# Performance work log

Hardware: AMD Instinct MI355X
Metric: run time of the kernel (lower is better)

Reference implementation:

```python
import jax, jax.numpy as jnp
import numpy as np

DIM = 4096
N_HEADS = 32
HEAD_DIM = DIM // N_HEADS  # 128
BSZ = 2
SEQLEN = 2048


def setup_inputs() -> dict:
    key = jax.random.key(0)
    ks = jax.random.split(key, 8)
    x = jax.random.normal(ks[0], (BSZ, SEQLEN, DIM), dtype=jnp.float32)
    # rotary frequencies (LLaMA): theta = 10000^{-2i/d}, angle = pos * theta
    inv_freq = 1.0 / (10000.0 ** (np.arange(0, HEAD_DIM, 2, dtype=np.float32) / HEAD_DIM))
    angles = np.arange(SEQLEN, dtype=np.float32)[:, None] * inv_freq[None, :]  # [S, hd/2]
    freqs_cos = jnp.asarray(np.cos(angles))
    freqs_sin = jnp.asarray(np.sin(angles))
    # causal additive mask [1,1,S,S]
    neg = jnp.float32(-1e9)
    mask = jnp.where(jnp.tril(jnp.ones((SEQLEN, SEQLEN), dtype=bool)), 0.0, neg)[None, None]
    scale = 0.02
    wq = jax.random.normal(ks[1], (DIM, DIM), dtype=jnp.float32) * scale
    wk = jax.random.normal(ks[2], (DIM, DIM), dtype=jnp.float32) * scale
    wv = jax.random.normal(ks[3], (DIM, DIM), dtype=jnp.float32) * scale
    wo = jax.random.normal(ks[4], (DIM, DIM), dtype=jnp.float32) * scale
    return {"x": x, "start_pos": 0, "freqs_cos": freqs_cos, "freqs_sin": freqs_sin,
            "mask": mask, "wq": wq, "wk": wk, "wv": wv, "wo": wo}


def _apply_rotary(t, cos, sin):
    # t: [B,S,H,hd]; cos/sin: [S,hd/2] -> broadcast [1,S,1,hd/2]
    t = t.reshape(*t.shape[:-1], HEAD_DIM // 2, 2)
    t0, t1 = t[..., 0], t[..., 1]
    c = cos[None, :, None, :]
    s = sin[None, :, None, :]
    r0 = t0 * c - t1 * s
    r1 = t0 * s + t1 * c
    return jnp.stack([r0, r1], axis=-1).reshape(*t0.shape[:-1], HEAD_DIM)


def reference(x, start_pos, freqs_cos, freqs_sin, mask, wq, wk, wv, wo):
    bsz, seqlen, _ = x.shape
    # QKV projections (nn.Linear: y = x @ W.T; weights stored [out,in])
    xq = (x @ wq.T).reshape(bsz, seqlen, N_HEADS, HEAD_DIM)
    xk = (x @ wk.T).reshape(bsz, seqlen, N_HEADS, HEAD_DIM)
    xv = (x @ wv.T).reshape(bsz, seqlen, N_HEADS, HEAD_DIM)
    xq = _apply_rotary(xq, freqs_cos, freqs_sin)
    xk = _apply_rotary(xk, freqs_cos, freqs_sin)
    # [B,H,S,hd]
    q = xq.transpose(0, 2, 1, 3)
    k = xk.transpose(0, 2, 1, 3)
    v = xv.transpose(0, 2, 1, 3)
    scale = 1.0 / jnp.sqrt(jnp.float32(HEAD_DIM))
    scores = jnp.einsum('bhqd,bhkd->bhqk', q, k) * scale + mask
    probs = jax.nn.softmax(scores, axis=-1)
    out = jnp.einsum('bhqk,bhkd->bhqd', probs, v)  # [B,H,S,hd]
    out = out.transpose(0, 2, 1, 3).reshape(bsz, seqlen, DIM)
    return out @ wo.T
```

## Files before the change

kernel.cpp:

```cpp
#include <hip/hip_runtime.h>

typedef unsigned short ushort_t;
typedef unsigned int u32;
typedef short bf16x8 __attribute__((ext_vector_type(8)));
typedef float f32x4 __attribute__((ext_vector_type(4)));
typedef float f32x16 __attribute__((ext_vector_type(16)));
typedef u32 u32x4 __attribute__((ext_vector_type(4)));

__device__ __forceinline__ ushort_t f2bf(float f) {
  u32 u = __builtin_bit_cast(u32, f);
  u += 0x7FFFu + ((u >> 16) & 1u);
  return (ushort_t)(u >> 16);
}
__device__ __forceinline__ float bf2f(u32 bits16) {
  return __builtin_bit_cast(float, bits16 << 16);
}

__global__ __launch_bounds__(256)
void cvt_kernel(const float* __restrict__ in, ushort_t* __restrict__ out) {
  const int i = blockIdx.x * 256 + threadIdx.x;
  const float4 a = ((const float4*)in)[(size_t)i * 2];
  const float4 b = ((const float4*)in)[(size_t)i * 2 + 1];
  uint4 r;
  r.x = (u32)f2bf(a.x) | ((u32)f2bf(a.y) << 16);
  r.y = (u32)f2bf(a.z) | ((u32)f2bf(a.w) << 16);
  r.z = (u32)f2bf(b.x) | ((u32)f2bf(b.y) << 16);
  r.w = (u32)f2bf(b.z) | ((u32)f2bf(b.w) << 16);
  ((uint4*)out)[i] = r;
}

template <int F32OUT>
__global__ __launch_bounds__(512, 2)
void gemm256(const ushort_t* __restrict__ A, const ushort_t* __restrict__ B,
             void* __restrict__ C) {
  constexpr int KD = 4096, ND = 4096;
  __shared__ ushort_t sA[2][2][128 * 64];
  __shared__ ushort_t sB[2][2][128 * 64];
  const int tid = threadIdx.x;
  const int lane = tid & 63, wave = tid >> 6;
  const int lq = lane & 15, g = lane >> 4;
  const int wm = wave >> 2, wn = wave & 3;
  const int id = blockIdx.x;
  const int swz = (id & 7) * 32 + (id >> 3);
  const int bm = (swz >> 4) * 256;
  const int bn = (swz & 15) * 256;
  const int csw = ((lane & 7) ^ (lane >> 3)) * 8;
  const int srow = lane >> 3;

  f32x4 acc[8][4];
#pragma unroll
  for (int m = 0; m < 8; ++m)
#pragma unroll
    for (int n = 0; n < 4; ++n) acc[m][n] = (f32x4)0.f;

#define STG(sbuf, G, rowb, t_, s_, h_)                                               \
  {                                                                                  \
    _Pragma("unroll") for (int i_ = 0; i_ < 2; ++i_) {                               \
      const int r0_ = wave * 16 + i_ * 8;                                            \
      const int tc_ = (t_) > 63 ? 63 : (t_);                                         \
      const ushort_t* src_ =                                                         \
          (G) + (size_t)((rowb) + (h_) * 128 + r0_ + srow) * KD + tc_ * 64 + csw;    \
      __builtin_amdgcn_global_load_lds(                                              \
          (const __attribute__((address_space(1))) u32*)src_,                        \
          (__attribute__((address_space(3))) u32*)&sbuf[s_][h_][r0_ * 64 + lane * 8],\
          16, 0, 0);                                                                 \
    }                                                                                \
  }
#define RD_A(S_, H_, mf_, kk_)                                                        \
  (*(const bf16x8*)&sA[S_][H_][(wm * 64 + (mf_) * 16 + lq) * 64 +                     \
                               ((((kk_) * 4 + g) ^ (lq & 7)) * 8)])
#define RD_B(S_, H_, nf_, kk_)                                                        \
  (*(const bf16x8*)&sB[S_][H_][(wn * 32 + (nf_) * 16 + lq) * 64 +                     \
                               ((((kk_) * 4 + g) ^ (lq & 7)) * 8)])
#define MM(MB, NB, BR)                                                                \
  _Pragma("unroll") for (int mf = 0; mf < 4; ++mf)                                    \
    _Pragma("unroll") for (int nf = 0; nf < 2; ++nf)                                  \
      _Pragma("unroll") for (int kk = 0; kk < 2; ++kk)                                \
        acc[(MB) + mf][(NB) + nf] = __builtin_amdgcn_mfma_f32_16x16x32_bf16(          \
            af[mf][kk], BR[nf][kk], acc[(MB) + mf][(NB) + nf], 0, 0, 0)

  STG(sA, A, bm, 0, 0, 0); STG(sA, A, bm, 0, 0, 1);
  STG(sB, B, bn, 0, 0, 0); STG(sB, B, bn, 0, 0, 1);
  STG(sA, A, bm, 1, 1, 0); STG(sA, A, bm, 1, 1, 1);
  STG(sB, B, bn, 1, 1, 1);
  asm volatile("s_waitcnt vmcnt(6)" ::: "memory");
  __builtin_amdgcn_s_barrier();
  __builtin_amdgcn_sched_barrier(0);

  bf16x8 af[4][2], b1[2][2], b0c[2][2], b0n[2][2];
#pragma unroll
  for (int nf = 0; nf < 2; ++nf)
#pragma unroll
    for (int kk = 0; kk < 2; ++kk) b0c[nf][kk] = RD_B(0, 0, nf, kk);

#define TILE(S_, T_, B0C, B0N)                                                        \
                                 \
  _Pragma("unroll") for (int mf = 0; mf < 4; ++mf)                                    \
    _Pragma("unroll") for (int kk = 0; kk < 2; ++kk)                                  \
      af[mf][kk] = RD_A(S_, 0, mf, kk);                                               \
  STG(sB, B, bn, (T_) + 1, (S_) ^ 1, 0);                                              \
  __builtin_amdgcn_s_barrier();                                                       \
  __builtin_amdgcn_s_setprio(1);                                                      \
  MM(0, 0, B0C);                                                                      \
  __builtin_amdgcn_s_setprio(0);                                                      \
  __builtin_amdgcn_s_barrier();                                                       \
                                                \
  _Pragma("unroll") for (int nf = 0; nf < 2; ++nf)                                    \
    _Pragma("unroll") for (int kk = 0; kk < 2; ++kk)                                  \
      b1[nf][kk] = RD_B(S_, 1, nf, kk);                                               \
  __builtin_amdgcn_s_barrier();                                                       \
  __builtin_amdgcn_s_setprio(1);                                                      \
  MM(0, 2, b1);                                                                       \
  __builtin_amdgcn_s_setprio(0);                                                      \
  __builtin_amdgcn_s_barrier();                                                       \
                                 \
  _Pragma("unroll") for (int mf = 0; mf < 4; ++mf)                                    \
    _Pragma("unroll") for (int kk = 0; kk < 2; ++kk)                                  \
      af[mf][kk] = RD_A(S_, 1, mf, kk);                                               \
  STG(sA, A, bm, (T_) + 2, S_, 0);                                                    \
  __builtin_amdgcn_s_barrier();                                                       \
  __builtin_amdgcn_s_setprio(1);                                                      \
  MM(4, 2, b1);                                                                       \
  __builtin_amdgcn_s_setprio(0);                                                      \
  __builtin_amdgcn_s_barrier();                                                       \
       \
  STG(sA, A, bm, (T_) + 2, S_, 1);                                                    \
  STG(sB, B, bn, (T_) + 2, S_, 1);                                                    \
  asm volatile("s_waitcnt vmcnt(6)" ::: "memory");                                    \
  __builtin_amdgcn_s_barrier();                                                       \
  __builtin_amdgcn_s_setprio(1);                                                      \
  MM(4, 0, B0C);                                                                      \
  __builtin_amdgcn_s_setprio(0);                                                      \
  _Pragma("unroll") for (int nf = 0; nf < 2; ++nf)                                    \
    _Pragma("unroll") for (int kk = 0; kk < 2; ++kk)                                  \
      B0N[nf][kk] = RD_B((S_) ^ 1, 0, nf, kk);                                        \
  __builtin_amdgcn_s_barrier();                                                       \
  __builtin_amdgcn_sched_barrier(0);

  for (int t = 0; t < 64; t += 2) {
    TILE(0, t, b0c, b0n)
    TILE(1, t + 1, b0n, b0c)
  }
#undef TILE
#undef STG
#undef RD_A
#undef RD_B
#undef MM

#pragma unroll
  for (int m = 0; m < 8; ++m) {
    const int grow = bm + (m >> 2) * 128 + wm * 64 + (m & 3) * 16 + g * 4;
#pragma unroll
    for (int r = 0; r < 4; ++r)
#pragma unroll
      for (int n = 0; n < 4; ++n) {
        const int gcol = bn + (n >> 1) * 128 + wn * 32 + (n & 1) * 16 + lq;
        if (F32OUT)
          ((float*)C)[(size_t)(grow + r) * ND + gcol] = acc[m][n][r];
        else
          ((ushort_t*)C)[(size_t)(grow + r) * ND + gcol] = f2bf(acc[m][n][r]);
      }
  }
}

__global__ __launch_bounds__(256)
void rope_kernel(ushort_t* __restrict__ Q, ushort_t* __restrict__ K,
                 const float* __restrict__ fcos, const float* __restrict__ fsin) {
  const int gid = blockIdx.x * 256 + threadIdx.x;
  ushort_t* T = blockIdx.y ? K : Q;
  const float scale = blockIdx.y ? 1.f : 0.08838834764831845f;
  const int j8 = gid & 15;
  const int h = (gid >> 4) & 31;
  const int s = (gid >> 9) & 2047;
  const int b = gid >> 20;
  const size_t off = (size_t)(b * 2048 + s) * 4096 + h * 128 + j8 * 8;
  uint4 v = *(const uint4*)(T + off);
  const float4 c4 = *(const float4*)(fcos + s * 64 + j8 * 4);
  const float4 s4 = *(const float4*)(fsin + s * 64 + j8 * 4);
  u32 w[4] = {v.x, v.y, v.z, v.w};
  const float cc[4] = {c4.x, c4.y, c4.z, c4.w};
  const float ss[4] = {s4.x, s4.y, s4.z, s4.w};
#pragma unroll
  for (int p = 0; p < 4; ++p) {
    const float t0 = bf2f(w[p] & 0xffffu);
    const float t1 = bf2f(w[p] >> 16);
    const float r0 = (t0 * cc[p] - t1 * ss[p]) * scale;
    const float r1 = (t0 * ss[p] + t1 * cc[p]) * scale;
    w[p] = (u32)f2bf(r0) | ((u32)f2bf(r1) << 16);
  }
  v.x = w[0]; v.y = w[1]; v.z = w[2]; v.w = w[3];
  *(uint4*)(T + off) = v;
}

__global__ __launch_bounds__(256, 2)
void attn_kernel(const ushort_t* __restrict__ Q, const ushort_t* __restrict__ K,
                 const ushort_t* __restrict__ Vt, ushort_t* __restrict__ O) {
  __shared__ ushort_t sK[2][32 * 128];
  __shared__ ushort_t sV[2][128 * 32];
  __shared__ float sScr[4][32];

  const int lane = threadIdx.x & 63, wave = threadIdx.x >> 6;
  const int lq = lane & 31, hi = lane >> 5;
  const int bp = blockIdx.x;
  const int bh = bp >> 3, j = bp & 7;
  const int h = bh & 31, b = bh >> 5;
  const ushort_t* Kb_ = K + (size_t)(b * 2048) * 4096 + h * 128;
  const ushort_t* Vb_ = Vt + (size_t)(h * 128) * 4096 + b * 2048;

#define STAGE(buf, kt_)                                                              \
  {                                                                                  \
    const int kb_ = (kt_) * 32;                                                      \
    _Pragma("unroll")                                                                \
    for (int i_ = 0; i_ < 2; ++i_) {                                                 \
      const int c_ = wave + i_ * 4;                                                  \
      const int krow = c_ * 4 + (lane >> 4);                                         \
      const int kcol = (lane & 15) ^ (krow & 7);                                     \
      const ushort_t* ksrc = Kb_ + (size_t)(kb_ + krow) * 4096 + kcol * 8;           \
      __builtin_amdgcn_global_load_lds(                                              \
          (const __attribute__((address_space(1))) u32*)ksrc,                        \
          (__attribute__((address_space(3))) u32*)&sK[buf][c_ * 512 + lane * 8],     \
          16, 0, 0);                                                                 \
      const int sst = c_ * 64 + lane;                                                \
      const int dv = sst >> 2;                                                       \
      const int gl = (sst & 3) ^ ((sst >> 3) & 3);                                   \
      const ushort_t* vsrc = Vb_ + (size_t)dv * 4096 + kb_ + gl * 8;                 \
      __builtin_amdgcn_global_load_lds(                                              \
          (const __attribute__((address_space(1))) u32*)vsrc,                        \
          (__attribute__((address_space(3))) u32*)&sV[buf][sst * 8], 16, 0, 0);      \
    }                                                                                \
  }

  for (int ph = 0; ph < 2; ++ph) {
    const int qj = ph ? (15 - j) : j;
    const int qbase = qj * 128 + wave * 32;
    const int ntw = qj * 4 + wave + 1;
    const int ntmax = qj * 4 + 4;

    bf16x8 aq[8];
    const ushort_t* qrow = Q + (size_t)(b * 2048 + qbase + lq) * 4096 + h * 128 + hi * 8;
#pragma unroll
    for (int kf = 0; kf < 8; ++kf) aq[kf] = *(const bf16x8*)(qrow + kf * 16);

    f32x16 o[4];
#pragma unroll
    for (int dt = 0; dt < 4; ++dt) o[dt] = (f32x16)0.f;
    float m_run = -1e30f, l_run = 0.f;

    int cur = 0;
    STAGE(0, 0);
    __syncthreads();

    for (int kt = 0; kt < ntmax; ++kt) {
      if (kt + 1 < ntmax) STAGE(cur ^ 1, kt + 1);
      if (kt < ntw) {
        const int kb = kt * 32;
        f32x16 st = (f32x16)0.f;
#pragma unroll
        for (int kf = 0; kf < 8; ++kf) {
          const bf16x8 kfrag =
              *(const bf16x8*)&sK[cur][lq * 128 + (((kf * 2 + hi) ^ (lq & 7)) * 8)];
          st = __builtin_amdgcn_mfma_f32_32x32x16_bf16(kfrag, aq[kf], st, 0, 0, 0);
        }
        if (kt == ntw - 1) {
          const int q = qbase + lq;
#pragma unroll
          for (int r = 0; r < 16; ++r) {
            const int key = kb + (r & 3) + 8 * (r >> 2) + 4 * hi;
            if (key > q) st[r] = -1e30f;
          }
        }
        float tm = st[0];
#pragma unroll
        for (int r = 1; r < 16; ++r) tm = fmaxf(tm, st[r]);
        tm = fmaxf(tm, __shfl_xor(tm, 32));
        if (!__all(tm <= m_run + 8.f)) {
          const float mnew = fmaxf(m_run, tm);
          const float corr = __expf(m_run - mnew);
          m_run = mnew;
          l_run *= corr;
          if (hi == 0) sScr[wave][lq] = corr;
          float fr[16];
#pragma unroll
          for (int r = 0; r < 16; ++r)
            fr[r] = sScr[wave][(r & 3) + 8 * (r >> 2) + 4 * hi];
#pragma unroll
          for (int dt = 0; dt < 4; ++dt)
#pragma unroll
            for (int r = 0; r < 16; ++r) o[dt][r] *= fr[r];
        }
        float rs = 0.f;
#pragma unroll
        for (int r = 0; r < 16; ++r) { st[r] = __expf(st[r] - m_run); rs += st[r]; }
        rs += __shfl_xor(rs, 32);
        l_run += rs;
        u32 A_, B_, C_, D_, E_, F_, G_, H_;
#define CVTPK(d_, l_, h_) \
  asm("v_cvt_pk_bf16_f32 %0, %1, %2" : "=v"(d_) : "v"(l_), "v"(h_))
        CVTPK(A_, st[0], st[1]);  CVTPK(B_, st[4], st[5]);
        CVTPK(C_, st[2], st[3]);  CVTPK(D_, st[6], st[7]);
        CVTPK(E_, st[8], st[9]);  CVTPK(F_, st[12], st[13]);
        CVTPK(G_, st[10], st[11]); CVTPK(H_, st[14], st[15]);
#undef CVTPK
        asm volatile("v_permlane32_swap_b32 %0, %1" : "+v"(A_), "+v"(B_));
        asm volatile("v_permlane32_swap_b32 %0, %1" : "+v"(C_), "+v"(D_));
        asm volatile("v_permlane32_swap_b32 %0, %1" : "+v"(E_), "+v"(F_));
        asm volatile("v_permlane32_swap_b32 %0, %1" : "+v"(G_), "+v"(H_));
        const bf16x8 pa0 = __builtin_bit_cast(bf16x8, (u32x4){A_, C_, B_, D_});
        const bf16x8 pa1 = __builtin_bit_cast(bf16x8, (u32x4){E_, G_, F_, H_});
#pragma unroll
        for (int dt = 0; dt < 4; ++dt) {
          const int d0 = dt * 32 + lq;
          const int s0 = 4 * d0 + ((hi + 0) ^ ((d0 >> 1) & 3));
          const int s1 = 4 * d0 + ((hi + 2) ^ ((d0 >> 1) & 3));
          const bf16x8 vf0 = *(const bf16x8*)&sV[cur][s0 * 8];
          const bf16x8 vf1 = *(const bf16x8*)&sV[cur][s1 * 8];
          o[dt] = __builtin_amdgcn_mfma_f32_32x32x16_bf16(pa0, vf0, o[dt], 0, 0, 0);
          o[dt] = __builtin_amdgcn_mfma_f32_32x32x16_bf16(pa1, vf1, o[dt], 0, 0, 0);
        }
      }
      __syncthreads();
      cur ^= 1;
    }

    if (hi == 0) sScr[wave][lq] = 1.f / l_run;
    __syncthreads();
    const size_t obase = (size_t)(b * 2048 + qbase) * 4096 + h * 128;
#pragma unroll
    for (int r = 0; r < 16; ++r) {
      const int qr = (r & 3) + 8 * (r >> 2) + 4 * hi;
      const float f = sScr[wave][qr];
#pragma unroll
      for (int dt = 0; dt < 4; ++dt)
        O[obase + (size_t)qr * 4096 + dt * 32 + lq] = f2bf(o[dt][r] * f);
    }
    __syncthreads();
  }
#undef STAGE
}

extern "C" void kernel_launch(void* const* d_in, const int* in_sizes, int n_in,
                              void* d_out, int out_size, void* d_ws, size_t ws_size,
                              hipStream_t stream) {
  const float* x = (const float*)d_in[0];
  const float* fcos = (const float*)d_in[2];
  const float* fsin = (const float*)d_in[3];
  const float* wq = (const float*)d_in[5];
  const float* wk = (const float*)d_in[6];
  const float* wv = (const float*)d_in[7];
  const float* wo = (const float*)d_in[8];
  float* out = (float*)d_out;
  char* ws = (char*)d_ws;
  const size_t MB32 = 33554432;
  ushort_t* xb = (ushort_t*)(ws);
  ushort_t* wb = (ushort_t*)(ws + MB32);
  ushort_t* Qb = (ushort_t*)(ws + 2 * MB32);
  ushort_t* Kb = (ushort_t*)(ws + 3 * MB32);
  ushort_t* Vt = (ushort_t*)(ws + 4 * MB32);
  ushort_t* Ob = xb;

  const dim3 cb(256);
  const dim3 cg(8192);
  const dim3 gb(512);
  const dim3 gg(256);

  hipLaunchKernelGGL(cvt_kernel, cg, cb, 0, stream, x, xb);
  hipLaunchKernelGGL(cvt_kernel, cg, cb, 0, stream, wq, wb);
  hipLaunchKernelGGL((gemm256<0>), gg, gb, 0, stream, xb, wb, (void*)Qb);
  hipLaunchKernelGGL(cvt_kernel, cg, cb, 0, stream, wk, wb);
  hipLaunchKernelGGL((gemm256<0>), gg, gb, 0, stream, xb, wb, (void*)Kb);
  hipLaunchKernelGGL(cvt_kernel, cg, cb, 0, stream, wv, wb);
  hipLaunchKernelGGL((gemm256<0>), gg, gb, 0, stream, wb, xb, (void*)Vt);
  hipLaunchKernelGGL(rope_kernel, dim3(8192, 2), cb, 0, stream, Qb, Kb, fcos, fsin);
  hipLaunchKernelGGL(attn_kernel, dim3(512), cb, 0, stream, Qb, Kb, Vt, Ob);
  hipLaunchKernelGGL(cvt_kernel, cg, cb, 0, stream, wo, wb);
  hipLaunchKernelGGL((gemm256<1>), gg, gb, 0, stream, Ob, wb, (void*)out);
}
```

Measured before the change: 679.5 us.

## Load B operand directly from global into registers, bypassing LDS staging

The GEMM no longer stages the B tile through shared memory. Each wave loads its B fragments straight from global memory into registers, prefetching one K-tile ahead, while A keeps the LDS double-buffered path. This halves LDS footprint and cuts the per-tile barrier phases from four to two. In exchange, B loads are uncoalesced per-lane 16-byte reads that are duplicated across the two wm waves, and the waitcnt accounting now has to cover the register loads. Out-of-range prefetches of A are redirected into a dump buffer.

```diff
diff --git a/kernel.cpp b/kernel.cpp
--- a/kernel.cpp
+++ b/kernel.cpp
@@ -35,7 +35,7 @@
              void* __restrict__ C) {
   constexpr int KD = 4096, ND = 4096;
   __shared__ ushort_t sA[2][2][128 * 64];
-  __shared__ ushort_t sB[2][2][128 * 64];
+  __shared__ ushort_t sDump[128 * 64];
   const int tid = threadIdx.x;
   const int lane = tid & 63, wave = tid >> 6;
   const int lq = lane & 15, g = lane >> 4;
@@ -47,104 +47,86 @@
   const int csw = ((lane & 7) ^ (lane >> 3)) * 8;
   const int srow = lane >> 3;
 
+  const ushort_t* Bb = B + (size_t)(bn + wn * 32 + lq) * KD + g * 8;
+  const ushort_t* Bp[4] = {Bb, Bb + (size_t)16 * KD, Bb + (size_t)128 * KD,
+                           Bb + (size_t)144 * KD};
+
   f32x4 acc[8][4];
 #pragma unroll
   for (int m = 0; m < 8; ++m)
 #pragma unroll
     for (int n = 0; n < 4; ++n) acc[m][n] = (f32x4)0.f;
 
-#define STG(sbuf, G, rowb, t_, s_, h_)                                               \
+#define STG(t_, s_, h_)                                                              \
   {                                                                                  \
     _Pragma("unroll") for (int i_ = 0; i_ < 2; ++i_) {                               \
       const int r0_ = wave * 16 + i_ * 8;                                            \
       const int tc_ = (t_) > 63 ? 63 : (t_);                                         \
       const ushort_t* src_ =                                                         \
-          (G) + (size_t)((rowb) + (h_) * 128 + r0_ + srow) * KD + tc_ * 64 + csw;    \
+          A + (size_t)(bm + (h_) * 128 + r0_ + srow) * KD + tc_ * 64 + csw;          \
+      ushort_t* d0_ = ((t_) < 64) ? &sA[s_][h_][r0_ * 64 + lane * 8]                 \
+                                  : &sDump[r0_ * 64 + lane * 8];                     \
       __builtin_amdgcn_global_load_lds(                                              \
           (const __attribute__((address_space(1))) u32*)src_,                        \
-          (__attribute__((address_space(3))) u32*)&sbuf[s_][h_][r0_ * 64 + lane * 8],\
-          16, 0, 0);                                                                 \
+          (__attribute__((address_space(3))) u32*)d0_, 16, 0, 0);                    \
     }                                                                                \
   }
 #define RD_A(S_, H_, mf_, kk_)                                                        \
   (*(const bf16x8*)&sA[S_][H_][(wm * 64 + (mf_) * 16 + lq) * 64 +                     \
                                ((((kk_) * 4 + g) ^ (lq & 7)) * 8)])
-#define RD_B(S_, H_, nf_, kk_)                                                        \
-  (*(const bf16x8*)&sB[S_][H_][(wn * 32 + (nf_) * 16 + lq) * 64 +                     \
-                               ((((kk_) * 4 + g) ^ (lq & 7)) * 8)])
-#define MM(MB, NB, BR)                                                                \
+#define LDB(BR, t_, n_, kk_)                                                          \
+  BR[n_][kk_] = *(const bf16x8*)(Bp[n_] + (((t_) > 63 ? 63 : (t_)) * 64 + (kk_) * 32))
+#define MM(MB, BR)                                                                    \
   _Pragma("unroll") for (int mf = 0; mf < 4; ++mf)                                    \
-    _Pragma("unroll") for (int nf = 0; nf < 2; ++nf)                                  \
+    _Pragma("unroll") for (int nf = 0; nf < 4; ++nf)                                  \
       _Pragma("unroll") for (int kk = 0; kk < 2; ++kk)                                \
-        acc[(MB) + mf][(NB) + nf] = __builtin_amdgcn_mfma_f32_16x16x32_bf16(          \
-            af[mf][kk], BR[nf][kk], acc[(MB) + mf][(NB) + nf], 0, 0, 0)
-
-  STG(sA, A, bm, 0, 0, 0); STG(sA, A, bm, 0, 0, 1);
-  STG(sB, B, bn, 0, 0, 0); STG(sB, B, bn, 0, 0, 1);
-  STG(sA, A, bm, 1, 1, 0); STG(sA, A, bm, 1, 1, 1);
-  STG(sB, B, bn, 1, 1, 1);
-  asm volatile("s_waitcnt vmcnt(6)" ::: "memory");
+        acc[(MB) + mf][nf] = __builtin_amdgcn_mfma_f32_16x16x32_bf16(                 \
+            af[mf][kk], BR[nf][kk], acc[(MB) + mf][nf], 0, 0, 0)
+
+  bf16x8 af[4][2], bcur[4][2], bnxt[4][2];
+
+#pragma unroll
+  for (int nf = 0; nf < 4; ++nf)
+#pragma unroll
+    for (int kk = 0; kk < 2; ++kk) LDB(bcur, 0, nf, kk);
+  STG(0, 0, 0); STG(0, 0, 1);
+  STG(1, 1, 0); STG(1, 1, 1);
+  asm volatile("s_waitcnt vmcnt(4)" ::: "memory");
   __builtin_amdgcn_s_barrier();
   __builtin_amdgcn_sched_barrier(0);
 
-  bf16x8 af[4][2], b1[2][2], b0c[2][2], b0n[2][2];
-#pragma unroll
-  for (int nf = 0; nf < 2; ++nf)
-#pragma unroll
-    for (int kk = 0; kk < 2; ++kk) b0c[nf][kk] = RD_B(0, 0, nf, kk);
-
-#define TILE(S_, T_, B0C, B0N)                                                        \
-                                 \
+#define TILE(S_, T_, BC, BN)                                                          \
   _Pragma("unroll") for (int mf = 0; mf < 4; ++mf)                                    \
     _Pragma("unroll") for (int kk = 0; kk < 2; ++kk)                                  \
       af[mf][kk] = RD_A(S_, 0, mf, kk);                                               \
-  STG(sB, B, bn, (T_) + 1, (S_) ^ 1, 0);                                              \
+  _Pragma("unroll") for (int nf = 0; nf < 4; ++nf)                                    \
+    _Pragma("unroll") for (int kk = 0; kk < 2; ++kk)                                  \
+      LDB(BN, (T_) + 1, nf, kk);                                                      \
   __builtin_amdgcn_s_barrier();                                                       \
   __builtin_amdgcn_s_setprio(1);                                                      \
-  MM(0, 0, B0C);                                                                      \
+  MM(0, BC);                                                                          \
   __builtin_amdgcn_s_setprio(0);                                                      \
   __builtin_amdgcn_s_barrier();                                                       \
-                                                \
-  _Pragma("unroll") for (int nf = 0; nf < 2; ++nf)                                    \
-    _Pragma("unroll") for (int kk = 0; kk < 2; ++kk)                                  \
-      b1[nf][kk] = RD_B(S_, 1, nf, kk);                                               \
-  __builtin_amdgcn_s_barrier();                                                       \
-  __builtin_amdgcn_s_setprio(1);                                                      \
-  MM(0, 2, b1);                                                                       \
-  __builtin_amdgcn_s_setprio(0);                                                      \
-  __builtin_amdgcn_s_barrier();                                                       \
-                                 \
   _Pragma("unroll") for (int mf = 0; mf < 4; ++mf)                                    \
     _Pragma("unroll") for (int kk = 0; kk < 2; ++kk)                                  \
       af[mf][kk] = RD_A(S_, 1, mf, kk);                                               \
-  STG(sA, A, bm, (T_) + 2, S_, 0);                                                    \
+  STG((T_) + 2, S_, 0);                                                               \
+  STG((T_) + 2, S_, 1);                                                               \
+  asm volatile("s_waitcnt vmcnt(12)" ::: "memory");                                   \
   __builtin_amdgcn_s_barrier();                                                       \
   __builtin_amdgcn_s_setprio(1);                                                      \
-  MM(4, 2, b1);                                                                       \
+  MM(4, BC);                                                                          \
   __builtin_amdgcn_s_setprio(0);                                                      \
-  __builtin_amdgcn_s_barrier();                                                       \
-       \
-  STG(sA, A, bm, (T_) + 2, S_, 1);                                                    \
-  STG(sB, B, bn, (T_) + 2, S_, 1);                                                    \
-  asm volatile("s_waitcnt vmcnt(6)" ::: "memory");                                    \
-  __builtin_amdgcn_s_barrier();                                                       \
-  __builtin_amdgcn_s_setprio(1);                                                      \
-  MM(4, 0, B0C);                                                                      \
-  __builtin_amdgcn_s_setprio(0);                                                      \
-  _Pragma("unroll") for (int nf = 0; nf < 2; ++nf)                                    \
-    _Pragma("unroll") for (int kk = 0; kk < 2; ++kk)                                  \
-      B0N[nf][kk] = RD_B((S_) ^ 1, 0, nf, kk);                                        \
-  __builtin_amdgcn_s_barrier();                                                       \
-  __builtin_amdgcn_sched_barrier(0);
+  __builtin_amdgcn_s_barrier();
 
   for (int t = 0; t < 64; t += 2) {
-    TILE(0, t, b0c, b0n)
-    TILE(1, t + 1, b0n, b0c)
+    TILE(0, t, bcur, bnxt)
+    TILE(1, t + 1, bnxt, bcur)
   }
 #undef TILE
 #undef STG
 #undef RD_A
-#undef RD_B
+#undef LDB
 #undef MM
 
 #pragma unroll
```

After: 944.2 us. +39.0%, slower.

## Simplify GEMM main loop to single-stage prefetch with one barrier per tile

Applied to the files above, without the earlier changes.

Replaces the finely interleaved ping-pong schedule (eight barriers per tile, staggered half-tile global-to-LDS loads two tiles ahead, cross-tile B register carry) with a simpler loop. Each iteration issues all loads for the next tile, reads both B halves and A halves from LDS, runs the MFMAs in two groups, then waits for all loads and synchronizes once. This cuts barrier count and register juggling, but the prefetch distance shrinks to one tile and vmcnt(0) exposes global load latency at the end of each tile.

```diff
diff --git a/kernel.cpp b/kernel.cpp
--- a/kernel.cpp
+++ b/kernel.cpp
@@ -72,80 +72,59 @@
 #define RD_B(S_, H_, nf_, kk_)                                                        \
   (*(const bf16x8*)&sB[S_][H_][(wn * 32 + (nf_) * 16 + lq) * 64 +                     \
                                ((((kk_) * 4 + g) ^ (lq & 7)) * 8)])
-#define MM(MB, NB, BR)                                                                \
+#define MM2(MB, B0R, B1R)                                                             \
   _Pragma("unroll") for (int mf = 0; mf < 4; ++mf)                                    \
     _Pragma("unroll") for (int nf = 0; nf < 2; ++nf)                                  \
-      _Pragma("unroll") for (int kk = 0; kk < 2; ++kk)                                \
-        acc[(MB) + mf][(NB) + nf] = __builtin_amdgcn_mfma_f32_16x16x32_bf16(          \
-            af[mf][kk], BR[nf][kk], acc[(MB) + mf][(NB) + nf], 0, 0, 0)
+      _Pragma("unroll") for (int kk = 0; kk < 2; ++kk) {                              \
+        acc[(MB) + mf][nf] = __builtin_amdgcn_mfma_f32_16x16x32_bf16(                 \
+            af[mf][kk], B0R[nf][kk], acc[(MB) + mf][nf], 0, 0, 0);                    \
+        acc[(MB) + mf][2 + nf] = __builtin_amdgcn_mfma_f32_16x16x32_bf16(             \
+            af[mf][kk], B1R[nf][kk], acc[(MB) + mf][2 + nf], 0, 0, 0);                \
+      }
 
   STG(sA, A, bm, 0, 0, 0); STG(sA, A, bm, 0, 0, 1);
   STG(sB, B, bn, 0, 0, 0); STG(sB, B, bn, 0, 0, 1);
-  STG(sA, A, bm, 1, 1, 0); STG(sA, A, bm, 1, 1, 1);
-  STG(sB, B, bn, 1, 1, 1);
-  asm volatile("s_waitcnt vmcnt(6)" ::: "memory");
+  asm volatile("s_waitcnt vmcnt(0)" ::: "memory");
   __builtin_amdgcn_s_barrier();
   __builtin_amdgcn_sched_barrier(0);
 
-  bf16x8 af[4][2], b1[2][2], b0c[2][2], b0n[2][2];
-#pragma unroll
-  for (int nf = 0; nf < 2; ++nf)
-#pragma unroll
-    for (int kk = 0; kk < 2; ++kk) b0c[nf][kk] = RD_B(0, 0, nf, kk);
-
-#define TILE(S_, T_, B0C, B0N)                                                        \
-                                 \
+  bf16x8 af[4][2], b0[2][2], b1[2][2];
+
+#define TILE(S_, T_)                                                                  \
+  STG(sA, A, bm, (T_) + 1, (S_) ^ 1, 0);                                              \
+  STG(sA, A, bm, (T_) + 1, (S_) ^ 1, 1);                                              \
+  STG(sB, B, bn, (T_) + 1, (S_) ^ 1, 0);                                              \
+  STG(sB, B, bn, (T_) + 1, (S_) ^ 1, 1);                                              \
   _Pragma("unroll") for (int mf = 0; mf < 4; ++mf)                                    \
     _Pragma("unroll") for (int kk = 0; kk < 2; ++kk)                                  \
       af[mf][kk] = RD_A(S_, 0, mf, kk);                                               \
-  STG(sB, B, bn, (T_) + 1, (S_) ^ 1, 0);                                              \
-  __builtin_amdgcn_s_barrier();                                                       \
+  _Pragma("unroll") for (int nf = 0; nf < 2; ++nf)                                    \
+    _Pragma("unroll") for (int kk = 0; kk < 2; ++kk) {                                \
+      b0[nf][kk] = RD_B(S_, 0, nf, kk);                                               \
+      b1[nf][kk] = RD_B(S_, 1, nf, kk);                                               \
+    }                                                                                 \
   __builtin_amdgcn_s_setprio(1);                                                      \
-  MM(0, 0, B0C);                                                                      \
+  MM2(0, b0, b1);                                                                     \
   __builtin_amdgcn_s_setprio(0);                                                      \
-  __builtin_amdgcn_s_barrier();                                                       \
-                                                \
-  _Pragma("unroll") for (int nf = 0; nf < 2; ++nf)                                    \
-    _Pragma("unroll") for (int kk = 0; kk < 2; ++kk)                                  \
-      b1[nf][kk] = RD_B(S_, 1, nf, kk);                                               \
-  __builtin_amdgcn_s_barrier();                                                       \
-  __builtin_amdgcn_s_setprio(1);                                                      \
-  MM(0, 2, b1);                                                                       \
-  __builtin_amdgcn_s_setprio(0);                                                      \
-  __builtin_amdgcn_s_barrier();                                                       \
-                                 \
   _Pragma("unroll") for (int mf = 0; mf < 4; ++mf)                                    \
     _Pragma("unroll") for (int kk = 0; kk < 2; ++kk)                                  \
       af[mf][kk] = RD_A(S_, 1, mf, kk);                                               \
-  STG(sA, A, bm, (T_) + 2, S_, 0);                                                    \
-  __builtin_amdgcn_s_barrier();                                                       \
   __builtin_amdgcn_s_setprio(1);                                                      \
-  MM(4, 2, b1);                                                                       \
+  MM2(4, b0, b1);                                                                     \
   __builtin_amdgcn_s_setprio(0);                                                      \
-  __builtin_amdgcn_s_barrier();                                                       \
-       \
-  STG(sA, A, bm, (T_) + 2, S_, 1);                                                    \
-  STG(sB, B, bn, (T_) + 2, S_, 1);                                                    \
-  asm volatile("s_waitcnt vmcnt(6)" ::: "memory");                                    \
-  __builtin_amdgcn_s_barrier();                                                       \
-  __builtin_amdgcn_s_setprio(1);                                                      \
-  MM(4, 0, B0C);                                                                      \
-  __builtin_amdgcn_s_setprio(0);                                                      \
-  _Pragma("unroll") for (int nf = 0; nf < 2; ++nf)                                    \
-    _Pragma("unroll") for (int kk = 0; kk < 2; ++kk)                                  \
-      B0N[nf][kk] = RD_B((S_) ^ 1, 0, nf, kk);                                        \
+  asm volatile("s_waitcnt vmcnt(0)" ::: "memory");                                    \
   __builtin_amdgcn_s_barrier();                                                       \
   __builtin_amdgcn_sched_barrier(0);
 
   for (int t = 0; t < 64; t += 2) {
-    TILE(0, t, b0c, b0n)
-    TILE(1, t + 1, b0n, b0c)
+    TILE(0, t)
+    TILE(1, t + 1)
   }
 #undef TILE
 #undef STG
 #undef RD_A
 #undef RD_B
-#undef MM
+#undef MM2
 
 #pragma unroll
   for (int m = 0; m < 8; ++m) {
```

Result: no change. 684.1 us (+0.7%).
